# Kernel optimization log

Hardware: AMD Instinct MI355X
Metric: run time of the kernel (lower is better)

The kernel has to match this reference:

```python
import jax, jax.numpy as jnp
import numpy as np

# dims
B, C, H, W = 2, 256, 128, 256
P, G = 9, 8            # num_pts, num_groups
GC = C // G            # group_channels


def setup_inputs() -> dict:
    key = jax.random.key(0)
    ks = jax.random.split(key, 8)
    s = 0.02
    return {
        "feats1": jax.random.normal(ks[0], (B, C, H, W), jnp.float32),
        "feats2": jax.random.normal(ks[1], (B, C, H, W), jnp.float32),
        "anchor_points": jax.random.uniform(ks[2], (B, H * W, 2), jnp.float32),
        "norm1_g": jnp.ones((C,), jnp.float32), "norm1_b": jnp.zeros((C,), jnp.float32),
        "norm2_g": jnp.ones((C,), jnp.float32), "norm2_b": jnp.zeros((C,), jnp.float32),
        "Wv": jax.random.normal(ks[3], (C, C), jnp.float32) * s, "bv": jnp.zeros((C,), jnp.float32),
        "Ww": jax.random.normal(ks[4], (C, G * P), jnp.float32) * s, "bw": jnp.zeros((G * P,), jnp.float32),
        "Wk": jax.random.normal(ks[5], (C, P), jnp.float32) * s, "bk": jnp.zeros((P,), jnp.float32),
        "Wo": jax.random.normal(ks[6], (C, C), jnp.float32) * s, "bo": jnp.zeros((C,), jnp.float32),
    }


def _ln(x, g, b):
    # LayerNorm over the last (channel) axis, eps as torch default
    m = jnp.mean(x, axis=-1, keepdims=True)
    v = jnp.mean(jnp.square(x - m), axis=-1, keepdims=True)
    return (x - m) * jax.lax.rsqrt(v + 1e-5) * g + b


def _bilinear_sample(value, pts):
    # value: (b, H, W, C); pts: (b, N, 2) normalized [0,1] (x, y)
    # grid_sample semantics: align_corners=False, zero padding
    b, h, w, c = value.shape
    x = pts[..., 0] * w - 0.5
    y = pts[..., 1] * h - 0.5
    x0 = jnp.floor(x)
    y0 = jnp.floor(y)
    wx = (x - x0)[..., None]
    wy = (y - y0)[..., None]
    x0i = x0.astype(jnp.int32)
    y0i = y0.astype(jnp.int32)
    vflat = value.reshape(b, h * w, c)

    def gather(yi, xi):
        valid = (yi >= 0) & (yi < h) & (xi >= 0) & (xi < w)
        idx = jnp.clip(yi, 0, h - 1) * w + jnp.clip(xi, 0, w - 1)
        g = jnp.take_along_axis(vflat, idx[..., None], axis=1)
        return g * valid[..., None].astype(value.dtype)

    v00 = gather(y0i, x0i)
    v01 = gather(y0i, x0i + 1)
    v10 = gather(y0i + 1, x0i)
    v11 = gather(y0i + 1, x0i + 1)
    return (v00 * (1 - wx) * (1 - wy) + v01 * wx * (1 - wy)
            + v10 * (1 - wx) * wy + v11 * wx * wy)


def reference(feats1, feats2, anchor_points, norm1_g, norm1_b, norm2_g, norm2_b,
              Wv, bv, Ww, bw, Wk, bk, Wo, bo):
    b, c, h, w = feats1.shape
    hw = h * w
    # to_3d(dim=2): (b, c, h, w) -> (b, hw, c); LayerNorm over c
    x1 = _ln(feats1.reshape(b, c, hw).transpose(0, 2, 1), norm1_g, norm1_b)
    x2 = _ln(feats2.reshape(b, c, hw).transpose(0, 2, 1), norm2_g, norm2_b)

    # value_proj (1x1 conv == per-pixel linear)
    value = (x2 @ Wv + bv).reshape(b, h, w, c)

    # weight_proj -> (b, hw, P, G); channel layout p*G + g; softmax over the P points per group
    logits = (x1 @ Ww + bw).reshape(b, hw, P, G)
    wts = jax.nn.softmax(logits, axis=2)

    # 1D key-point generator: per-pixel learned offsets along x around the anchor
    off = x1 @ Wk + bk                                   # (b, hw, P) normalized offsets
    kx = anchor_points[..., 0:1] + off                   # (b, hw, P)
    ky = jnp.broadcast_to(anchor_points[..., 1:2], kx.shape)
    kp = jnp.stack([kx, ky], axis=-1)                    # (b, hw, P, 2)

    # deformable aggregation: bilinear gather + group-weighted sum over points
    samp = _bilinear_sample(value, kp.reshape(b, hw * P, 2)).reshape(b, hw, P, G, GC)
    agg = jnp.einsum('bnpgc,bnpg->bngc', samp, wts).reshape(b, hw, c)

    out = (agg @ Wo + bo).reshape(b, h, w, c).transpose(0, 3, 1, 2)  # (b, c, h, w)
    return out, kp.reshape(b, h, w, P, 2)
```

## Files before the change

### kernel.cpp

```cpp
#include <hip/hip_runtime.h>
#include <hip/hip_bf16.h>


constexpr int B = 2, C = 256, H = 128, W = 256;
constexpr int HW = H * W;
constexpr int P = 9, G = 8;
constexpr int PIX = 32;
constexpr int NPIX = B * HW;
constexpr int NBKT = 2 * 129;

typedef __attribute__((ext_vector_type(8))) __bf16 bf16x8;
typedef __attribute__((ext_vector_type(4))) float f32x4;

static __device__ __forceinline__ unsigned short f2bf(float x) {
    __hip_bfloat16 h = __float2bfloat16(x);
    return *reinterpret_cast<unsigned short*>(&h);
}
static __device__ __forceinline__ unsigned int pack2(float a, float b) {
    return (unsigned int)f2bf(a) | ((unsigned int)f2bf(b) << 16);
}
static __device__ __forceinline__ float bf2f(unsigned short u) {
    return __uint_as_float((unsigned int)u << 16);
}
static __device__ __forceinline__ bf16x8 ldb8g(const unsigned short* p) {
    return *reinterpret_cast<const bf16x8*>(p);
}

__global__ __launch_bounds__(256) void k_prep(
    const float* __restrict__ Ww, const float* __restrict__ Wv,
    const float* __restrict__ Wo,
    unsigned short* __restrict__ WwT, unsigned short* __restrict__ WvT,
    unsigned short* __restrict__ WoT)
{
    int tid = blockIdx.x * 256 + threadIdx.x;
    if (tid < 20480) {
        int n = tid >> 8, k = tid & 255;
        WwT[tid] = f2bf((n < 72) ? Ww[k * 72 + n] : 0.f);
    } else if (tid < 20480 + 65536) {
        int i = tid - 20480;
        int n = i >> 8, k = i & 255;
        WvT[i] = f2bf(Wv[k * 256 + n]);
    } else {
        int i = tid - 86016;
        int n = i >> 8, k = i & 255;
        WoT[i] = f2bf(Wo[k * 256 + n]);
    }
}

static __device__ __forceinline__ int bucket_of(const float* anchor, int pix) {
    float ay = anchor[(size_t)pix * 2 + 1];
    int y0 = (int)floorf(ay * (float)H - 0.5f);
    y0 = min(max(y0, -1), H - 1);
    return (pix >> 15) * 129 + y0 + 1;
}

__global__ __launch_bounds__(256) void k_hist(
    const float* __restrict__ anchor, int* __restrict__ hist)
{
    int pix = blockIdx.x * 256 + threadIdx.x;
    atomicAdd(&hist[bucket_of(anchor, pix)], 1);
}

__global__ __launch_bounds__(256) void k_scan(
    const int* __restrict__ hist, int* __restrict__ cursor)
{
    __shared__ int h[NBKT];
    int t = threadIdx.x;
    for (int i = t; i < NBKT; i += 256) h[i] = hist[i];
    __syncthreads();
    if (t == 0) {
        int run = 0;
        for (int i = 0; i < NBKT; ++i) { int v = h[i]; cursor[i] = run; run += v; }
    }
}

__global__ __launch_bounds__(256) void k_scatter(
    const float* __restrict__ anchor, int* __restrict__ cursor,
    int* __restrict__ perm)
{
    int pix = blockIdx.x * 256 + threadIdx.x;
    int pos = atomicAdd(&cursor[bucket_of(anchor, pix)], 1);
    perm[pos] = pix;
}

__global__ __launch_bounds__(256) void kA(
    const float* __restrict__ feats1, const float* __restrict__ anchor,
    const float* __restrict__ g1, const float* __restrict__ b1,
    const float* __restrict__ Wk, const float* __restrict__ bk,
    const unsigned short* __restrict__ WwT, const float* __restrict__ bw,
    unsigned short* __restrict__ wtsb, float* __restrict__ kp_out)
{
    __shared__ unsigned short Hi[PIX][264];
    __shared__ __align__(16) char smB[20480];
    __shared__ float meanA[PIX], rstdA[PIX], axL[PIX], ayL[PIX];

    float* WkL  = (float*)smB;
    float* red2 = (float*)(smB + 9216);
    float* red  = (float*)(smB + 18432);
    float* Lg   = (float*)smB;

    const int t = threadIdx.x;
    const int p = t & 31;
    const int part = t >> 5;
    const int gpix0 = blockIdx.x * PIX;
    const int b = gpix0 >> 15;
    const int n0 = gpix0 & (HW - 1);
    const float* Fb = feats1 + (size_t)b * C * HW;

    for (int i = t; i < 2304; i += 256) WkL[i] = Wk[i];
    if (t < PIX) {
        axL[t] = anchor[((size_t)gpix0 + t) * 2 + 0];
        ayL[t] = anchor[((size_t)gpix0 + t) * 2 + 1];
    }

    float x[32];
    #pragma unroll
    for (int i = 0; i < 32; ++i)
        x[i] = Fb[(size_t)(part * 32 + i) * HW + n0 + p];

    float s = 0.f, ss = 0.f;
    #pragma unroll
    for (int i = 0; i < 32; ++i) { s += x[i]; ss += x[i] * x[i]; }
    red[part * 32 + p] = s;
    red[256 + part * 32 + p] = ss;
    __syncthreads();
    if (part == 0) {
        float s2 = 0.f, ss2 = 0.f;
        #pragma unroll
        for (int k = 0; k < 8; ++k) { s2 += red[k * 32 + p]; ss2 += red[256 + k * 32 + p]; }
        float mean = s2 * (1.f / C);
        float var  = ss2 * (1.f / C) - mean * mean;
        meanA[p] = mean; rstdA[p] = rsqrtf(var + 1e-5f);
    }
    __syncthreads();

    {
        float mean = meanA[p], rstd = rstdA[p];
        #pragma unroll
        for (int i = 0; i < 32; ++i) {
            int c = part * 32 + i;
            x[i] = (x[i] - mean) * rstd * g1[c] + b1[c];
        }
    }

    {
        float po[9];
        #pragma unroll
        for (int pt = 0; pt < 9; ++pt) po[pt] = 0.f;
        #pragma unroll 4
        for (int i = 0; i < 32; ++i) {
            int c = part * 32 + i;
            float xv = x[i];
            #pragma unroll
            for (int pt = 0; pt < 9; ++pt) po[pt] += xv * WkL[c * 9 + pt];
        }
        #pragma unroll
        for (int pt = 0; pt < 9; ++pt) red2[(part * 32 + p) * 9 + pt] = po[pt];
    }

    {
        unsigned int* row = (unsigned int*)&Hi[p][part * 32];
        #pragma unroll
        for (int i = 0; i < 16; ++i) row[i] = pack2(x[2 * i], x[2 * i + 1]);
    }
    __syncthreads();

    for (int tau = t; tau < 288; tau += 256) {
        int px = tau & 31, pt = tau >> 5;
        float off = bk[pt];
        #pragma unroll
        for (int k = 0; k < 8; ++k) off += red2[(k * 32 + px) * 9 + pt];
        size_t o = (((size_t)gpix0 + px) * P + pt) * 2;
        kp_out[o] = axL[px] + off;
        kp_out[o + 1] = ayL[px];
    }

    const int wave = t >> 6, lane = t & 63;
    const int l15 = lane & 15, quad = lane >> 4;
    const int mt = wave & 1;
    const int ntb = (wave >> 1) * 3;
    const int ntc = (wave >> 1) ? 2 : 3;

    f32x4 acc[3];
    #pragma unroll
    for (int j = 0; j < 3; ++j) acc[j] = (f32x4){0.f, 0.f, 0.f, 0.f};

    const unsigned short* arow = &Hi[mt * 16 + l15][quad * 8];
    for (int kk = 0; kk < 8; ++kk) {
        bf16x8 a = *reinterpret_cast<const bf16x8*>(arow + kk * 32);
        for (int j = 0; j < 3; ++j) {
            if (j < ntc) {
                bf16x8 bfr = ldb8g(WwT + (size_t)((ntb + j) * 16 + l15) * 256 + quad * 8 + kk * 32);
                acc[j] = __builtin_amdgcn_mfma_f32_16x16x32_bf16(a, bfr, acc[j], 0, 0, 0);
            }
        }
    }
    __syncthreads();

    #pragma unroll
    for (int j = 0; j < 3; ++j) {
        if (j < ntc) {
            int n = (ntb + j) * 16 + l15;
            if (n < 72) {
                float bwn = bw[n];
                #pragma unroll
                for (int r = 0; r < 4; ++r)
                    Lg[(mt * 16 + quad * 4 + r) * 81 + n] = acc[j][r] + bwn;
            }
        }
    }
    __syncthreads();

    {
        int px = t >> 3, g = t & 7;
        float m = -1e30f;
        #pragma unroll
        for (int pt = 0; pt < P; ++pt) m = fmaxf(m, Lg[px * 81 + pt * 8 + g]);
        float e[P], sum = 0.f;
        #pragma unroll
        for (int pt = 0; pt < P; ++pt) { e[pt] = __expf(Lg[px * 81 + pt * 8 + g] - m); sum += e[pt]; }
        float inv = 1.f / sum;
        unsigned short* wb = wtsb + ((size_t)gpix0 + px) * 72 + g * 9;
        #pragma unroll
        for (int pt = 0; pt < P; ++pt) wb[pt] = f2bf(e[pt] * inv);
    }
}

__global__ __launch_bounds__(256) void kB(
    const float* __restrict__ feats2,
    const float* __restrict__ g2, const float* __restrict__ b2,
    const unsigned short* __restrict__ WvT, const float* __restrict__ bv,
    unsigned short* __restrict__ val)
{
    __shared__ unsigned short Hi[PIX][264];
    __shared__ float red[2][8][PIX];
    __shared__ float meanA[PIX], rstdA[PIX];

    const int t = threadIdx.x;
    const int p = t & 31;
    const int part = t >> 5;
    const int gpix0 = blockIdx.x * PIX;
    const int b = gpix0 >> 15;
    const int n0 = gpix0 & (HW - 1);
    const float* Fb = feats2 + (size_t)b * C * HW;

    float x[32];
    #pragma unroll
    for (int i = 0; i < 32; ++i)
        x[i] = Fb[(size_t)(part * 32 + i) * HW + n0 + p];

    float s = 0.f, ss = 0.f;
    #pragma unroll
    for (int i = 0; i < 32; ++i) { s += x[i]; ss += x[i] * x[i]; }
    red[0][part][p] = s; red[1][part][p] = ss;
    __syncthreads();
    if (part == 0) {
        float s2 = 0.f, ss2 = 0.f;
        #pragma unroll
        for (int k = 0; k < 8; ++k) { s2 += red[0][k][p]; ss2 += red[1][k][p]; }
        float mean = s2 * (1.f / C);
        float var  = ss2 * (1.f / C) - mean * mean;
        meanA[p] = mean; rstdA[p] = rsqrtf(var + 1e-5f);
    }
    __syncthreads();
    {
        float mean = meanA[p], rstd = rstdA[p];
        unsigned int* row = (unsigned int*)&Hi[p][part * 32];
        #pragma unroll
        for (int i = 0; i < 16; ++i) {
            float v0 = (x[2 * i] - mean) * rstd * g2[part * 32 + 2 * i] + b2[part * 32 + 2 * i];
            float v1 = (x[2 * i + 1] - mean) * rstd * g2[part * 32 + 2 * i + 1] + b2[part * 32 + 2 * i + 1];
            row[i] = pack2(v0, v1);
        }
    }
    __syncthreads();

    const int wave = t >> 6, lane = t & 63;
    const int l15 = lane & 15, quad = lane >> 4;
    const int m0 = wave * 64;

    f32x4 acc[4][2];
    #pragma unroll
    for (int ms = 0; ms < 4; ++ms)
        #pragma unroll
        for (int nt = 0; nt < 2; ++nt)
            acc[ms][nt] = (f32x4){0.f, 0.f, 0.f, 0.f};

    for (int kk = 0; kk < 8; ++kk) {
        bf16x8 a[4], bfr[2];
        #pragma unroll
        for (int ms = 0; ms < 4; ++ms)
            a[ms] = ldb8g(WvT + (size_t)(m0 + ms * 16 + l15) * 256 + quad * 8 + kk * 32);
        #pragma unroll
        for (int nt = 0; nt < 2; ++nt)
            bfr[nt] = *reinterpret_cast<const bf16x8*>(&Hi[nt * 16 + l15][quad * 8 + kk * 32]);
        #pragma unroll
        for (int ms = 0; ms < 4; ++ms)
            #pragma unroll
            for (int nt = 0; nt < 2; ++nt)
                acc[ms][nt] = __builtin_amdgcn_mfma_f32_16x16x32_bf16(a[ms], bfr[nt], acc[ms][nt], 0, 0, 0);
    }

    #pragma unroll
    for (int ms = 0; ms < 4; ++ms) {
        int ch0 = m0 + ms * 16 + quad * 4;
        float b0 = bv[ch0], b1v = bv[ch0 + 1], b2v = bv[ch0 + 2], b3 = bv[ch0 + 3];
        #pragma unroll
        for (int nt = 0; nt < 2; ++nt) {
            int pix = gpix0 + nt * 16 + l15;
            uint2 o;
            o.x = pack2(acc[ms][nt][0] + b0, acc[ms][nt][1] + b1v);
            o.y = pack2(acc[ms][nt][2] + b2v, acc[ms][nt][3] + b3);
            *reinterpret_cast<uint2*>(val + (size_t)pix * 256 + ch0) = o;
        }
    }
}

__global__ __launch_bounds__(256) void k_gather(
    const unsigned short* __restrict__ wtsb,
    const float* __restrict__ kp,
    const unsigned short* __restrict__ val,
    const int* __restrict__ perm,
    unsigned short* __restrict__ aggb)
{
    __shared__ float Wl[PIX][72];
    __shared__ float KPl[PIX][18];
    __shared__ int pixL[PIX];

    const int t = threadIdx.x;
    const int gpix0 = blockIdx.x * PIX;

    if (t < PIX) pixL[t] = perm[gpix0 + t];
    __syncthreads();

    {
        int px = t >> 3, j = t & 7;
        int pix = pixL[px];
        const unsigned short* wrow = wtsb + (size_t)pix * 72 + j * 9;
        #pragma unroll
        for (int k = 0; k < 9; ++k) Wl[px][j * 9 + k] = bf2f(wrow[k]);
        const float* krow = kp + (size_t)pix * 18;
        for (int k = j; k < 18; k += 8) KPl[px][k] = krow[k];
    }
    __syncthreads();

    const int wave = t >> 6, lane = t & 63;
    const int gl = lane >> 3;

    for (int px = wave; px < PIX; px += 4) {
        const int pix = pixL[px];
        const unsigned short* vbp = val + ((size_t)(pix >> 15) * HW) * 256 + 4 * lane;

        const float ay = KPl[px][1];
        float yf = ay * (float)H - 0.5f;
        float y0f = floorf(yf);
        float wy = yf - y0f;
        int y0 = (int)y0f;
        float vy0 = ((unsigned)y0 < (unsigned)H) ? 1.f : 0.f;
        float vy1 = ((unsigned)(y0 + 1) < (unsigned)H) ? 1.f : 0.f;
        int y0c = min(max(y0, 0), H - 1);
        int y1c = min(max(y0 + 1, 0), H - 1);

        float a0 = 0.f, a1 = 0.f, a2 = 0.f, a3 = 0.f;

        #pragma unroll
        for (int pt = 0; pt < P; ++pt) {
            float kx = KPl[px][2 * pt];
            float w  = Wl[px][gl * 9 + pt];
            float xf = kx * (float)W - 0.5f;
            float x0f = floorf(xf);
            float wx = xf - x0f;
            int x0 = (int)x0f;
            float vx0 = ((unsigned)x0 < (unsigned)W) ? 1.f : 0.f;
            float vx1 = ((unsigned)(x0 + 1) < (unsigned)W) ? 1.f : 0.f;
            int x0c = min(max(x0, 0), W - 1);
            int x1c = min(max(x0 + 1, 0), W - 1);

            float c00 = w * (1.f - wx) * (1.f - wy) * vy0 * vx0;
            float c01 = w * wx * (1.f - wy) * vy0 * vx1;
            float c10 = w * (1.f - wx) * wy * vy1 * vx0;
            float c11 = w * wx * wy * vy1 * vx1;

            uint2 u00 = *(const uint2*)(vbp + ((size_t)(y0c * W + x0c) << 8));
            uint2 u01 = *(const uint2*)(vbp + ((size_t)(y0c * W + x1c) << 8));
            uint2 u10 = *(const uint2*)(vbp + ((size_t)(y1c * W + x0c) << 8));
            uint2 u11 = *(const uint2*)(vbp + ((size_t)(y1c * W + x1c) << 8));

            a0 += c00 * __uint_as_float(u00.x << 16) + c01 * __uint_as_float(u01.x << 16)
                + c10 * __uint_as_float(u10.x << 16) + c11 * __uint_as_float(u11.x << 16);
            a1 += c00 * __uint_as_float(u00.x & 0xffff0000u) + c01 * __uint_as_float(u01.x & 0xffff0000u)
                + c10 * __uint_as_float(u10.x & 0xffff0000u) + c11 * __uint_as_float(u11.x & 0xffff0000u);
            a2 += c00 * __uint_as_float(u00.y << 16) + c01 * __uint_as_float(u01.y << 16)
                + c10 * __uint_as_float(u10.y << 16) + c11 * __uint_as_float(u11.y << 16);
            a3 += c00 * __uint_as_float(u00.y & 0xffff0000u) + c01 * __uint_as_float(u01.y & 0xffff0000u)
                + c10 * __uint_as_float(u10.y & 0xffff0000u) + c11 * __uint_as_float(u11.y & 0xffff0000u);
        }

        uint2 o;
        o.x = pack2(a0, a1);
        o.y = pack2(a2, a3);
        *reinterpret_cast<uint2*>(aggb + ((size_t)pix << 8) + 4 * lane) = o;
    }
}

__global__ __launch_bounds__(256) void k_gemmo(
    const unsigned short* __restrict__ aggb,
    const unsigned short* __restrict__ WoT,
    const float* __restrict__ bo,
    float* __restrict__ out)
{
    const int t = threadIdx.x;
    const int wave = t >> 6, lane = t & 63;
    const int n_base = blockIdx.x * 64;
    const int b = n_base >> 15;
    const int hw0 = n_base & (HW - 1);
    const int m0 = wave * 64;
    const int l15 = lane & 15, quad = lane >> 4;

    f32x4 acc[4][4];
    #pragma unroll
    for (int ms = 0; ms < 4; ++ms)
        #pragma unroll
        for (int ns = 0; ns < 4; ++ns)
            acc[ms][ns] = (f32x4){0.f, 0.f, 0.f, 0.f};

    size_t aoff[4], boff[4];
    #pragma unroll
    for (int ms = 0; ms < 4; ++ms)
        aoff[ms] = (size_t)(m0 + ms * 16 + l15) * 256 + quad * 8;
    #pragma unroll
    for (int ns = 0; ns < 4; ++ns)
        boff[ns] = (size_t)(n_base + ns * 16 + l15) * 256 + quad * 8;

    for (int kk = 0; kk < 8; ++kk) {
        bf16x8 a[4], bfr[4];
        #pragma unroll
        for (int ms = 0; ms < 4; ++ms) a[ms] = ldb8g(WoT + aoff[ms] + kk * 32);
        #pragma unroll
        for (int ns = 0; ns < 4; ++ns) bfr[ns] = ldb8g(aggb + boff[ns] + kk * 32);
        #pragma unroll
        for (int ms = 0; ms < 4; ++ms)
            #pragma unroll
            for (int ns = 0; ns < 4; ++ns)
                acc[ms][ns] = __builtin_amdgcn_mfma_f32_16x16x32_bf16(a[ms], bfr[ns], acc[ms][ns], 0, 0, 0);
    }

    float bor[4][4];
    #pragma unroll
    for (int ms = 0; ms < 4; ++ms)
        #pragma unroll
        for (int r = 0; r < 4; ++r)
            bor[ms][r] = bo[m0 + ms * 16 + quad * 4 + r];

    #pragma unroll
    for (int ms = 0; ms < 4; ++ms) {
        #pragma unroll
        for (int ns = 0; ns < 4; ++ns) {
            #pragma unroll
            for (int r = 0; r < 4; ++r) {
                int ch = m0 + ms * 16 + quad * 4 + r;
                out[((size_t)b * 256 + ch) * HW + hw0 + ns * 16 + l15] = acc[ms][ns][r] + bor[ms][r];
            }
        }
    }
}

extern "C" void kernel_launch(void* const* d_in, const int* in_sizes, int n_in,
                              void* d_out, int out_size, void* d_ws, size_t ws_size,
                              hipStream_t stream)
{
    const float* feats1 = (const float*)d_in[0];
    const float* feats2 = (const float*)d_in[1];
    const float* anchor = (const float*)d_in[2];
    const float* n1g    = (const float*)d_in[3];
    const float* n1b    = (const float*)d_in[4];
    const float* n2g    = (const float*)d_in[5];
    const float* n2b    = (const float*)d_in[6];
    const float* Wv     = (const float*)d_in[7];
    const float* bv     = (const float*)d_in[8];
    const float* Ww     = (const float*)d_in[9];
    const float* bw     = (const float*)d_in[10];
    const float* Wk     = (const float*)d_in[11];
    const float* bk     = (const float*)d_in[12];
    const float* Wo     = (const float*)d_in[13];
    const float* bo     = (const float*)d_in[14];

    float* out = (float*)d_out;
    float* kp  = out + (size_t)B * C * HW;

    char* ws = (char*)d_ws;
    unsigned short* val  = (unsigned short*)(ws);
    unsigned short* aggb = (unsigned short*)(ws + 33554432);
    unsigned short* wtsb = (unsigned short*)(ws + 67108864);
    unsigned short* WwT  = (unsigned short*)(ws + 76546048);
    unsigned short* WvT  = (unsigned short*)(ws + 76587008);
    unsigned short* WoT  = (unsigned short*)(ws + 76718080);
    int* perm   = (int*)(ws + 76849152);
    int* hist   = (int*)(ws + 77111296);
    int* cursor = hist + NBKT;

    hipMemsetAsync(hist, 0, NBKT * sizeof(int), stream);
    k_prep   <<<592,  256, 0, stream>>>(Ww, Wv, Wo, WwT, WvT, WoT);
    k_hist   <<<256,  256, 0, stream>>>(anchor, hist);
    k_scan   <<<1,    256, 0, stream>>>(hist, cursor);
    k_scatter<<<256,  256, 0, stream>>>(anchor, cursor, perm);
    kA       <<<2048, 256, 0, stream>>>(feats1, anchor, n1g, n1b, Wk, bk, WwT, bw, wtsb, kp);
    kB       <<<2048, 256, 0, stream>>>(feats2, n2g, n2b, WvT, bv, val);
    k_gather <<<2048, 256, 0, stream>>>(wtsb, kp, val, perm, aggb);
    k_gemmo  <<<1024, 256, 0, stream>>>(aggb, WoT, bo, out);
}
```

Baseline: 479.6 us.

## Localize histogram/scatter atomics, remap gather blocks across XCDs, pack FMAs

The bucket histogram and scatter now count with per-block shared-memory atomics. A two-level scan builds per-block offsets, which removes global atomic contention and the memset. The gather kernel remaps block indices so that consecutive sorted pixel tiles land on the same XCD (phys&7 stride), aiming for better L2 reuse of value rows. The bilinear inner loop factors the corner weights and accumulates with float2 vectors to enable packed FMA. The ordering within buckets changes, but the result is still deterministic in membership.

```diff
diff --git a/kernel.cpp b/kernel.cpp
--- a/kernel.cpp
+++ b/kernel.cpp
@@ -11,6 +11,7 @@
 
 typedef __attribute__((ext_vector_type(8))) __bf16 bf16x8;
 typedef __attribute__((ext_vector_type(4))) float f32x4;
+typedef __attribute__((ext_vector_type(2))) float f32x2;
 
 static __device__ __forceinline__ unsigned short f2bf(float x) {
     __hip_bfloat16 h = __float2bfloat16(x);
@@ -54,32 +55,54 @@
     return (pix >> 15) * 129 + y0 + 1;
 }
 
-__global__ __launch_bounds__(256) void k_hist(
-    const float* __restrict__ anchor, int* __restrict__ hist)
-{
-    int pix = blockIdx.x * 256 + threadIdx.x;
-    atomicAdd(&hist[bucket_of(anchor, pix)], 1);
+__global__ __launch_bounds__(1024) void k_hist(
+    const float* __restrict__ anchor, int* __restrict__ hist64)
+{
+    __shared__ int h[NBKT];
+    const int t = threadIdx.x, blk = blockIdx.x;
+    for (int i = t; i < NBKT; i += 1024) h[i] = 0;
+    __syncthreads();
+    atomicAdd(&h[bucket_of(anchor, blk * 1024 + t)], 1);
+    __syncthreads();
+    for (int i = t; i < NBKT; i += 1024) hist64[blk * NBKT + i] = h[i];
 }
 
 __global__ __launch_bounds__(256) void k_scan(
-    const int* __restrict__ hist, int* __restrict__ cursor)
-{
-    __shared__ int h[NBKT];
-    int t = threadIdx.x;
-    for (int i = t; i < NBKT; i += 256) h[i] = hist[i];
+    const int* __restrict__ hist64, int* __restrict__ off)
+{
+    __shared__ int tot[NBKT], base[NBKT];
+    const int t = threadIdx.x;
+    for (int bkt = t; bkt < NBKT; bkt += 256) {
+        int run = 0;
+        for (int blk = 0; blk < 64; ++blk) run += hist64[blk * NBKT + bkt];
+        tot[bkt] = run;
+    }
     __syncthreads();
     if (t == 0) {
         int run = 0;
-        for (int i = 0; i < NBKT; ++i) { int v = h[i]; cursor[i] = run; run += v; }
-    }
-}
-
-__global__ __launch_bounds__(256) void k_scatter(
-    const float* __restrict__ anchor, int* __restrict__ cursor,
+        for (int i = 0; i < NBKT; ++i) { base[i] = run; run += tot[i]; }
+    }
+    __syncthreads();
+    for (int bkt = t; bkt < NBKT; bkt += 256) {
+        int run = base[bkt];
+        for (int blk = 0; blk < 64; ++blk) {
+            int v = hist64[blk * NBKT + bkt];
+            off[blk * NBKT + bkt] = run;
+            run += v;
+        }
+    }
+}
+
+__global__ __launch_bounds__(1024) void k_scatter(
+    const float* __restrict__ anchor, const int* __restrict__ off,
     int* __restrict__ perm)
 {
-    int pix = blockIdx.x * 256 + threadIdx.x;
-    int pos = atomicAdd(&cursor[bucket_of(anchor, pix)], 1);
+    __shared__ int cur[NBKT];
+    const int t = threadIdx.x, blk = blockIdx.x;
+    for (int i = t; i < NBKT; i += 1024) cur[i] = off[blk * NBKT + i];
+    __syncthreads();
+    int pix = blk * 1024 + t;
+    int pos = atomicAdd(&cur[bucket_of(anchor, pix)], 1);
     perm[pos] = pix;
 }
 
@@ -167,11 +190,11 @@
 
     for (int tau = t; tau < 288; tau += 256) {
         int px = tau & 31, pt = tau >> 5;
-        float off = bk[pt];
-        #pragma unroll
-        for (int k = 0; k < 8; ++k) off += red2[(k * 32 + px) * 9 + pt];
+        float offv = bk[pt];
+        #pragma unroll
+        for (int k = 0; k < 8; ++k) offv += red2[(k * 32 + px) * 9 + pt];
         size_t o = (((size_t)gpix0 + px) * P + pt) * 2;
-        kp_out[o] = axL[px] + off;
+        kp_out[o] = axL[px] + offv;
         kp_out[o + 1] = ayL[px];
     }
 
@@ -328,7 +351,9 @@
     __shared__ int pixL[PIX];
 
     const int t = threadIdx.x;
-    const int gpix0 = blockIdx.x * PIX;
+    const int phys = blockIdx.x;
+    const int lb = (phys & 7) * 256 + (phys >> 3);
+    const int gpix0 = lb * PIX;
 
     if (t < PIX) pixL[t] = perm[gpix0 + t];
     __syncthreads();
@@ -356,12 +381,13 @@
         float y0f = floorf(yf);
         float wy = yf - y0f;
         int y0 = (int)y0f;
-        float vy0 = ((unsigned)y0 < (unsigned)H) ? 1.f : 0.f;
-        float vy1 = ((unsigned)(y0 + 1) < (unsigned)H) ? 1.f : 0.f;
-        int y0c = min(max(y0, 0), H - 1);
-        int y1c = min(max(y0 + 1, 0), H - 1);
-
-        float a0 = 0.f, a1 = 0.f, a2 = 0.f, a3 = 0.f;
+        float e0 = (((unsigned)y0 < (unsigned)H) ? 1.f : 0.f) * (1.f - wy);
+        float e1 = (((unsigned)(y0 + 1) < (unsigned)H) ? 1.f : 0.f) * wy;
+        int yb0 = min(max(y0, 0), H - 1) * W;
+        int yb1 = min(max(y0 + 1, 0), H - 1) * W;
+
+        f32x2 a01 = (f32x2){0.f, 0.f};
+        f32x2 a23 = (f32x2){0.f, 0.f};
 
         #pragma unroll
         for (int pt = 0; pt < P; ++pt) {
@@ -371,34 +397,40 @@
             float x0f = floorf(xf);
             float wx = xf - x0f;
             int x0 = (int)x0f;
-            float vx0 = ((unsigned)x0 < (unsigned)W) ? 1.f : 0.f;
-            float vx1 = ((unsigned)(x0 + 1) < (unsigned)W) ? 1.f : 0.f;
+            float t0 = w * (1.f - wx) * (((unsigned)x0 < (unsigned)W) ? 1.f : 0.f);
+            float t1 = w * wx * (((unsigned)(x0 + 1) < (unsigned)W) ? 1.f : 0.f);
             int x0c = min(max(x0, 0), W - 1);
             int x1c = min(max(x0 + 1, 0), W - 1);
 
-            float c00 = w * (1.f - wx) * (1.f - wy) * vy0 * vx0;
-            float c01 = w * wx * (1.f - wy) * vy0 * vx1;
-            float c10 = w * (1.f - wx) * wy * vy1 * vx0;
-            float c11 = w * wx * wy * vy1 * vx1;
-
-            uint2 u00 = *(const uint2*)(vbp + ((size_t)(y0c * W + x0c) << 8));
-            uint2 u01 = *(const uint2*)(vbp + ((size_t)(y0c * W + x1c) << 8));
-            uint2 u10 = *(const uint2*)(vbp + ((size_t)(y1c * W + x0c) << 8));
-            uint2 u11 = *(const uint2*)(vbp + ((size_t)(y1c * W + x1c) << 8));
-
-            a0 += c00 * __uint_as_float(u00.x << 16) + c01 * __uint_as_float(u01.x << 16)
-                + c10 * __uint_as_float(u10.x << 16) + c11 * __uint_as_float(u11.x << 16);
-            a1 += c00 * __uint_as_float(u00.x & 0xffff0000u) + c01 * __uint_as_float(u01.x & 0xffff0000u)
-                + c10 * __uint_as_float(u10.x & 0xffff0000u) + c11 * __uint_as_float(u11.x & 0xffff0000u);
-            a2 += c00 * __uint_as_float(u00.y << 16) + c01 * __uint_as_float(u01.y << 16)
-                + c10 * __uint_as_float(u10.y << 16) + c11 * __uint_as_float(u11.y << 16);
-            a3 += c00 * __uint_as_float(u00.y & 0xffff0000u) + c01 * __uint_as_float(u01.y & 0xffff0000u)
-                + c10 * __uint_as_float(u10.y & 0xffff0000u) + c11 * __uint_as_float(u11.y & 0xffff0000u);
+            float c00 = t0 * e0, c01 = t1 * e0, c10 = t0 * e1, c11 = t1 * e1;
+
+            uint2 u00 = *(const uint2*)(vbp + ((size_t)(yb0 + x0c) << 8));
+            uint2 u01 = *(const uint2*)(vbp + ((size_t)(yb0 + x1c) << 8));
+            uint2 u10 = *(const uint2*)(vbp + ((size_t)(yb1 + x0c) << 8));
+            uint2 u11 = *(const uint2*)(vbp + ((size_t)(yb1 + x1c) << 8));
+
+            f32x2 v;
+            v.x = __uint_as_float(u00.x << 16); v.y = __uint_as_float(u00.x & 0xffff0000u);
+            a01 += v * c00;
+            v.x = __uint_as_float(u00.y << 16); v.y = __uint_as_float(u00.y & 0xffff0000u);
+            a23 += v * c00;
+            v.x = __uint_as_float(u01.x << 16); v.y = __uint_as_float(u01.x & 0xffff0000u);
+            a01 += v * c01;
+            v.x = __uint_as_float(u01.y << 16); v.y = __uint_as_float(u01.y & 0xffff0000u);
+            a23 += v * c01;
+            v.x = __uint_as_float(u10.x << 16); v.y = __uint_as_float(u10.x & 0xffff0000u);
+            a01 += v * c10;
+            v.x = __uint_as_float(u10.y << 16); v.y = __uint_as_float(u10.y & 0xffff0000u);
+            a23 += v * c10;
+            v.x = __uint_as_float(u11.x << 16); v.y = __uint_as_float(u11.x & 0xffff0000u);
+            a01 += v * c11;
+            v.x = __uint_as_float(u11.y << 16); v.y = __uint_as_float(u11.y & 0xffff0000u);
+            a23 += v * c11;
         }
 
         uint2 o;
-        o.x = pack2(a0, a1);
-        o.y = pack2(a2, a3);
+        o.x = pack2(a01.x, a01.y);
+        o.y = pack2(a23.x, a23.y);
         *reinterpret_cast<uint2*>(aggb + ((size_t)pix << 8) + 4 * lane) = o;
     }
 }
@@ -496,16 +528,15 @@
     unsigned short* WvT  = (unsigned short*)(ws + 76587008);
     unsigned short* WoT  = (unsigned short*)(ws + 76718080);
     int* perm   = (int*)(ws + 76849152);
-    int* hist   = (int*)(ws + 77111296);
-    int* cursor = hist + NBKT;
-
-    hipMemsetAsync(hist, 0, NBKT * sizeof(int), stream);
-    k_prep   <<<592,  256, 0, stream>>>(Ww, Wv, Wo, WwT, WvT, WoT);
-    k_hist   <<<256,  256, 0, stream>>>(anchor, hist);
-    k_scan   <<<1,    256, 0, stream>>>(hist, cursor);
-    k_scatter<<<256,  256, 0, stream>>>(anchor, cursor, perm);
-    kA       <<<2048, 256, 0, stream>>>(feats1, anchor, n1g, n1b, Wk, bk, WwT, bw, wtsb, kp);
-    kB       <<<2048, 256, 0, stream>>>(feats2, n2g, n2b, WvT, bv, val);
-    k_gather <<<2048, 256, 0, stream>>>(wtsb, kp, val, perm, aggb);
-    k_gemmo  <<<1024, 256, 0, stream>>>(aggb, WoT, bo, out);
-}
+    int* hist64 = (int*)(ws + 77111296);
+    int* off    = (int*)(ws + 77375488);
+
+    k_prep   <<<592,  256,  0, stream>>>(Ww, Wv, Wo, WwT, WvT, WoT);
+    k_hist   <<<64,   1024, 0, stream>>>(anchor, hist64);
+    k_scan   <<<1,    256,  0, stream>>>(hist64, off);
+    k_scatter<<<64,   1024, 0, stream>>>(anchor, off, perm);
+    kA       <<<2048, 256,  0, stream>>>(feats1, anchor, n1g, n1b, Wk, bk, WwT, bw, wtsb, kp);
+    kB       <<<2048, 256,  0, stream>>>(feats2, n2g, n2b, WvT, bv, val);
+    k_gather <<<2048, 256,  0, stream>>>(wtsb, kp, val, perm, aggb);
+    k_gemmo  <<<1024, 256,  0, stream>>>(aggb, WoT, bo, out);
+}
```

New measurement: 406.9 us. 1.18x faster.
